# Optimization experiments

Hardware: AMD Instinct MI355X
Metric: run time of the kernel (lower is better)

Reference implementation:

```python
import jax, jax.numpy as jnp
import numpy as np

N_NODES = 100000
N_EDGES = 3200000
N_GRAPHS = 2048
DIM = 32
FEAT = 78
OUT = 128
BN_EPS = 1e-5


def setup_inputs() -> dict:
    key = jax.random.key(0)
    ks = jax.random.split(key, 16)
    x = jax.random.normal(ks[0], (N_NODES, FEAT), dtype=jnp.float32)
    edge_index = jax.random.randint(ks[1], (2, N_EDGES), 0, N_NODES, dtype=jnp.int64)
    batch = jnp.sort(jax.random.randint(ks[2], (N_NODES,), 0, N_GRAPHS, dtype=jnp.int64))
    s = 0.1
    # layer 1 MLP (78 -> 32 -> 32)
    W1a = jax.random.normal(ks[3], (FEAT, DIM), dtype=jnp.float32) * s
    b1a = jnp.zeros((DIM,), jnp.float32)
    W1b = jax.random.normal(ks[4], (DIM, DIM), dtype=jnp.float32) * s
    b1b = jnp.zeros((DIM,), jnp.float32)
    # layers 2-5 MLPs stacked (32 -> 32 -> 32)
    Wa = jax.random.normal(ks[5], (4, DIM, DIM), dtype=jnp.float32) * s
    ba = jnp.zeros((4, DIM), jnp.float32)
    Wb = jax.random.normal(ks[6], (4, DIM, DIM), dtype=jnp.float32) * s
    bb = jnp.zeros((4, DIM), jnp.float32)
    # batchnorm affine params for 5 layers
    gamma = jnp.ones((5, DIM), jnp.float32)
    beta = jnp.zeros((5, DIM), jnp.float32)
    # final graph-level linear 32 -> 128
    Wfc = jax.random.normal(ks[7], (DIM, OUT), dtype=jnp.float32) * s
    bfc = jnp.zeros((OUT,), jnp.float32)
    return {"x": x, "edge_index": edge_index, "batch": batch,
            "W1a": W1a, "b1a": b1a, "W1b": W1b, "b1b": b1b,
            "Wa": Wa, "ba": ba, "Wb": Wb, "bb": bb,
            "gamma": gamma, "beta": beta, "Wfc": Wfc, "bfc": bfc}


def _gin_layer(h, edge_index, Wa, ba, Wb, bb, g, b):
    # GIN aggregation (eps=0): h_i + sum_{j->i} h_j via scatter-add on dst
    src, dst = edge_index[0], edge_index[1]
    agg = h + jax.ops.segment_sum(h[src], dst, num_segments=h.shape[0])
    # tiny MLP: Linear -> ReLU -> Linear
    h = jax.nn.relu(agg @ Wa + ba) @ Wb + bb
    h = jax.nn.relu(h)
    # BatchNorm1d (training mode, biased variance)
    mu = h.mean(axis=0)
    var = ((h - mu) ** 2).mean(axis=0)
    return (h - mu) * jax.lax.rsqrt(var + BN_EPS) * g + b


def reference(x, edge_index, batch, W1a, b1a, W1b, b1b, Wa, ba, Wb, bb, gamma, beta, Wfc, bfc):
    h = _gin_layer(x, edge_index, W1a, b1a, W1b, b1b, gamma[0], beta[0])
    for i in range(4):
        h = _gin_layer(h, edge_index, Wa[i], ba[i], Wb[i], bb[i], gamma[i + 1], beta[i + 1])
    # global_add_pool over graphs
    pooled = jax.ops.segment_sum(h, batch, num_segments=N_GRAPHS)  # [G, 32]
    out = jax.nn.relu(pooled @ Wfc + bfc)  # dropout = identity in eval
    return out
```

## Files before the change

### kernel.cpp

```cpp
#include <hip/hip_runtime.h>
#include <hip/hip_fp16.h>

#define N_NODES 100000
#define N_GRAPHS 2048
#define N_EDGES 3200000
#define NHALF 50000
#define DIM 32
#define FEAT 78
#define OUT_DIM 128
#define BN_EPS 1e-5f

#define BSHIFT 9
#define BSIZE 512
#define NB ((N_NODES + BSIZE - 1) / BSIZE)
#define CHUNK 4096
#define NSUB 4
#define NR 4

#define NTILES (N_NODES / 16)
#define SBINS 64
#define AGG_BLOCKS 3128

typedef _Float16 f16x8 __attribute__((ext_vector_type(8)));
typedef float f32x4 __attribute__((ext_vector_type(4)));

__global__ __launch_bounds__(256) void bucket_hist_kernel(const int* __restrict__ dst,
                                                          int* __restrict__ bcnt) {
    __shared__ int lh[256];
    int tid = threadIdx.x;
    lh[tid] = 0;
    __syncthreads();
    const int4* d4 = (const int4*)dst;
    const int n4 = N_EDGES / 4;
    int i = blockIdx.x * blockDim.x + tid;
    int stride = gridDim.x * blockDim.x;
    for (; i < n4; i += stride) {
        int4 v = d4[i];
        atomicAdd(&lh[v.x >> BSHIFT], 1);
        atomicAdd(&lh[v.y >> BSHIFT], 1);
        atomicAdd(&lh[v.z >> BSHIFT], 1);
        atomicAdd(&lh[v.w >> BSHIFT], 1);
    }
    __syncthreads();
    if (tid < NB && lh[tid])
        atomicAdd(&bcnt[tid], lh[tid]);
}

__global__ __launch_bounds__(256) void bucket_scan_kernel(const int* __restrict__ bcnt,
                                                          int* __restrict__ bstart,
                                                          int* __restrict__ bcursor,
                                                          int* __restrict__ rowst) {
    __shared__ int sc[256];
    int tid = threadIdx.x;
    int v = (tid < NB) ? bcnt[tid] : 0;
    sc[tid] = v;
    __syncthreads();
    for (int off = 1; off < 256; off <<= 1) {
        int nv = (tid >= off) ? sc[tid - off] : 0;
        __syncthreads();
        sc[tid] += nv;
        __syncthreads();
    }
    if (tid < NB) {
        int ex = sc[tid] - v;
        bstart[tid] = ex;
        bcursor[tid] = ex;
    }
    if (tid == 0) {
        bstart[NB] = N_EDGES;
        rowst[N_NODES] = N_EDGES;
    }
}

__global__ __launch_bounds__(256) void bucket_scatter_kernel(const int* __restrict__ src,
                                                             const int* __restrict__ dst,
                                                             int* __restrict__ bcursor,
                                                             int* __restrict__ epk) {
    __shared__ int lpk[CHUNK];
    __shared__ unsigned char lbkt[CHUNK];
    __shared__ int lhist[4 * 256];
    __shared__ int lwcur[4 * 256];
    __shared__ int sc[256];
    __shared__ int lpre[256];
    __shared__ int gbase[256];
    int tid = threadIdx.x;
    int wave = tid >> 6;
    int base = blockIdx.x * CHUNK;
    int n = N_EDGES - base; if (n > CHUNK) n = CHUNK;

    for (int j = tid; j < 4 * 256; j += 256) lhist[j] = 0;
    __syncthreads();
    for (int i = tid; i < n; i += 256)
        atomicAdd(&lhist[wave * 256 + (dst[base + i] >> BSHIFT)], 1);
    __syncthreads();
    int c0 = lhist[0 * 256 + tid];
    int c1 = lhist[1 * 256 + tid];
    int c2 = lhist[2 * 256 + tid];
    int c3 = lhist[3 * 256 + tid];
    int v = c0 + c1 + c2 + c3;
    sc[tid] = v;
    __syncthreads();
    for (int off = 1; off < 256; off <<= 1) {
        int nv = (tid >= off) ? sc[tid - off] : 0;
        __syncthreads();
        sc[tid] += nv;
        __syncthreads();
    }
    int ex = sc[tid] - v;
    lpre[tid] = ex;
    lwcur[0 * 256 + tid] = ex;
    lwcur[1 * 256 + tid] = ex + c0;
    lwcur[2 * 256 + tid] = ex + c0 + c1;
    lwcur[3 * 256 + tid] = ex + c0 + c1 + c2;
    if (tid < NB && v)
        gbase[tid] = atomicAdd(&bcursor[tid], v);
    __syncthreads();
    for (int i = tid; i < n; i += 256) {
        int d = dst[base + i];
        int s = src[base + i];
        int b = d >> BSHIFT;
        int pos = atomicAdd(&lwcur[wave * 256 + b], 1);
        lpk[pos] = ((d & (BSIZE - 1)) << 17) | s;
        lbkt[pos] = (unsigned char)b;
    }
    __syncthreads();
    for (int i = tid; i < n; i += 256) {
        int b = lbkt[i];
        int gpos = gbase[b] + (i - lpre[b]);
        epk[gpos] = lpk[i];
    }
}

__global__ __launch_bounds__(256) void node_count_kernel(const int* __restrict__ bstart,
                                                         const int* __restrict__ epk,
                                                         int* __restrict__ qcnt) {
    __shared__ int lcnt[4 * BSIZE];
    int tid = threadIdx.x;
    int wave = tid >> 6;
    int b = blockIdx.x / NSUB;
    int qt = blockIdx.x % NSUB;
    int ss = bstart[b], se = bstart[b + 1];
    int len = se - ss;
    int qs = ss + (int)(((long long)len * qt) / NSUB);
    int qe = ss + (int)(((long long)len * (qt + 1)) / NSUB);
    for (int j = tid; j < 4 * BSIZE; j += 256) lcnt[j] = 0;
    __syncthreads();
    for (int i = qs + tid; i < qe; i += 256) {
        int pk = epk[i];
        int add = 0x10000 | (((pk & 0x1FFFF) < NHALF) ? 1 : 0);
        atomicAdd(&lcnt[wave * BSIZE + (pk >> 17)], add);
    }
    __syncthreads();
    int* qc = qcnt + (size_t)blockIdx.x * BSIZE;
    qc[tid] = lcnt[tid] + lcnt[BSIZE + tid] + lcnt[2 * BSIZE + tid] + lcnt[3 * BSIZE + tid];
    int t2 = tid + 256;
    qc[t2] = lcnt[t2] + lcnt[BSIZE + t2] + lcnt[2 * BSIZE + t2] + lcnt[3 * BSIZE + t2];
}

__global__ __launch_bounds__(256) void node_scan_kernel(const int* __restrict__ bstart,
                                                        const int* __restrict__ qcnt,
                                                        int* __restrict__ qbase0,
                                                        int* __restrict__ qbase1,
                                                        int* __restrict__ rowst,
                                                        int* __restrict__ rowmid,
                                                        float* __restrict__ degf) {
    __shared__ int sc[256];
    int tid = threadIdx.x;
    int b = blockIdx.x;
    int ss = bstart[b];
    const int* qc = qcnt + (size_t)b * NSUB * BSIZE;
    int j0 = 2 * tid, j1 = 2 * tid + 1;
    int pk0[NSUB], pk1[NSUB];
    int t0 = 0, t1 = 0, m0 = 0, m1 = 0;
    #pragma unroll
    for (int q = 0; q < NSUB; ++q) {
        pk0[q] = qc[q * BSIZE + j0];
        pk1[q] = qc[q * BSIZE + j1];
        t0 += pk0[q] >> 16; m0 += pk0[q] & 0xFFFF;
        t1 += pk1[q] >> 16; m1 += pk1[q] & 0xFFFF;
    }
    int s = t0 + t1;
    sc[tid] = s;
    __syncthreads();
    for (int off = 1; off < 256; off <<= 1) {
        int nv = (tid >= off) ? sc[tid - off] : 0;
        __syncthreads();
        sc[tid] += nv;
        __syncthreads();
    }
    int ex = sc[tid] - s;
    int B0 = ss + ex;
    int B1 = B0 + t0;
    int node_base = b << BSHIFT;
    if (node_base + j0 < N_NODES) {
        rowst[node_base + j0] = B0; rowmid[node_base + j0] = B0 + m0;
        degf[node_base + j0] = (float)(t0 + 1);
    }
    if (node_base + j1 < N_NODES) {
        rowst[node_base + j1] = B1; rowmid[node_base + j1] = B1 + m1;
        degf[node_base + j1] = (float)(t1 + 1);
    }
    int r0a = B0, r0b = B0 + m0;
    int r1a = B1, r1b = B1 + m1;
    #pragma unroll
    for (int q = 0; q < NSUB; ++q) {
        int c0 = pk0[q] & 0xFFFF, ct = pk0[q] >> 16;
        qbase0[((size_t)b * NSUB + q) * BSIZE + j0] = r0a; r0a += c0;
        qbase1[((size_t)b * NSUB + q) * BSIZE + j0] = r0b; r0b += ct - c0;
        int d0c = pk1[q] & 0xFFFF, dt = pk1[q] >> 16;
        qbase0[((size_t)b * NSUB + q) * BSIZE + j1] = r1a; r1a += d0c;
        qbase1[((size_t)b * NSUB + q) * BSIZE + j1] = r1b; r1b += dt - d0c;
    }
}

__global__ __launch_bounds__(256) void node_scatter_kernel(const int* __restrict__ bstart,
                                                           const int* __restrict__ epk,
                                                           const int* __restrict__ qbase0,
                                                           const int* __restrict__ qbase1,
                                                           int* __restrict__ csr) {
    __shared__ int lcur[2 * NSUB * 128];
    int tid = threadIdx.x;
    int b = blockIdx.x / NR;
    int r = blockIdx.x % NR;
    for (int j = tid; j < NSUB * 128; j += 256) {
        int q = j >> 7, n = j & 127;
        lcur[j] = qbase0[((size_t)b * NSUB + q) * BSIZE + r * 128 + n];
        lcur[NSUB * 128 + j] = qbase1[((size_t)b * NSUB + q) * BSIZE + r * 128 + n];
    }
    __syncthreads();
    int ss = bstart[b], se = bstart[b + 1];
    int len = se - ss;
    #pragma unroll
    for (int q = 0; q < NSUB; ++q) {
        int qs = ss + (int)(((long long)len * q) / NSUB);
        int qe = ss + (int)(((long long)len * (q + 1)) / NSUB);
        for (int i = qs + tid; i < qe; i += 256) {
            int pk = epk[i];
            int nloc = pk >> 17;
            if ((nloc >> 7) == r) {
                int s = pk & 0x1FFFF;
                int h = (s >= NHALF) ? NSUB * 128 : 0;
                int pos = atomicAdd(&lcur[h + (q << 7) + (nloc & 127)], 1);
                csr[pos] = s;
            }
        }
    }
}

__global__ __launch_bounds__(1024) void prep0_kernel(const float* __restrict__ W1a,
                                                     const float* __restrict__ W1b,
                                                     __half* __restrict__ blob1,
                                                     __half* __restrict__ blob,
                                                     float* __restrict__ cwf) {
    int tid = threadIdx.x;
    for (int idx = tid; idx < 6 * 512; idx += 1024) {
        int e = idx & 7;
        int l = (idx >> 3) & 63;
        int f = idx >> 9;
        int kc = f >> 1, ct = f & 1;
        int k = kc * 32 + (l >> 4) * 8 + e;
        int col = ct * 16 + (l & 15);
        float v = (k < FEAT) ? W1a[k * DIM + col] : 0.f;
        blob1[idx] = __float2half(v);
    }
    int d = tid >> 5, k = tid & 31;
    blob[d * 32 + k] = __float2half((d == k) ? 1.f : 0.f);
    blob[1024 + d * 32 + k] = __float2half(W1b[k * 32 + d]);
    if (tid < DIM) cwf[tid] = 0.f;
}

__global__ __launch_bounds__(256) void transform1_kernel(const float* __restrict__ x,
                                                         const __half* __restrict__ blob1,
                                                         __half* __restrict__ T) {
    __shared__ __align__(16) _Float16 X[4][512];
    int tid = threadIdx.x;
    int wave = tid >> 6;
    int l = tid & 63;
    int d0 = l & 15, kg = l >> 4;
    int tile = blockIdx.x * 4 + wave;
    if (tile >= NTILES) return;
    int tb = tile * 16;
    const float* xr = x + (size_t)(tb + d0) * FEAT;

    f16x8 af0, af1, af2;
    #pragma unroll
    for (int j = 0; j < 4; ++j) {
        int k0 = kg * 8 + 2 * j;
        float2 v0 = *(const float2*)(xr + k0);
        float2 v1 = *(const float2*)(xr + 32 + k0);
        af0[2 * j] = (_Float16)v0.x; af0[2 * j + 1] = (_Float16)v0.y;
        af1[2 * j] = (_Float16)v1.x; af1[2 * j + 1] = (_Float16)v1.y;
        int k2 = 64 + k0;
        float2 v2 = {0.f, 0.f};
        if (k2 < FEAT) v2 = *(const float2*)(xr + k2);
        af2[2 * j] = (_Float16)v2.x; af2[2 * j + 1] = (_Float16)v2.y;
    }
    f16x8 b0 = *(const f16x8*)(blob1 + (0 * 64 + l) * 8);
    f16x8 b1 = *(const f16x8*)(blob1 + (1 * 64 + l) * 8);
    f16x8 b2 = *(const f16x8*)(blob1 + (2 * 64 + l) * 8);
    f16x8 b3 = *(const f16x8*)(blob1 + (3 * 64 + l) * 8);
    f16x8 b4 = *(const f16x8*)(blob1 + (4 * 64 + l) * 8);
    f16x8 b5 = *(const f16x8*)(blob1 + (5 * 64 + l) * 8);

    f32x4 c0 = {0.f, 0.f, 0.f, 0.f};
    f32x4 c1 = {0.f, 0.f, 0.f, 0.f};
    c0 = __builtin_amdgcn_mfma_f32_16x16x32_f16(af0, b0, c0, 0, 0, 0);
    c1 = __builtin_amdgcn_mfma_f32_16x16x32_f16(af0, b1, c1, 0, 0, 0);
    c0 = __builtin_amdgcn_mfma_f32_16x16x32_f16(af1, b2, c0, 0, 0, 0);
    c1 = __builtin_amdgcn_mfma_f32_16x16x32_f16(af1, b3, c1, 0, 0, 0);
    c0 = __builtin_amdgcn_mfma_f32_16x16x32_f16(af2, b4, c0, 0, 0, 0);
    c1 = __builtin_amdgcn_mfma_f32_16x16x32_f16(af2, b5, c1, 0, 0, 0);

    #pragma unroll
    for (int rr = 0; rr < 4; ++rr) {
        int row = kg * 4 + rr;
        X[wave][row * 32 + d0] = (_Float16)c0[rr];
        X[wave][row * 32 + d0 + 16] = (_Float16)c1[rr];
    }
    __builtin_amdgcn_wave_barrier();
    int gg = l >> 2, cq = l & 3;
    uint4 vv = *(uint4*)&X[wave][gg * 32 + cq * 8];
    *(uint4*)(T + (size_t)(tb + gg) * DIM + cq * 8) = vv;
}

__global__ __launch_bounds__(1024) void prep_kernel(const float* __restrict__ sbins,
                                                    const float* __restrict__ gamma,
                                                    const float* __restrict__ beta,
                                                    const float* __restrict__ Wa,
                                                    const float* __restrict__ Wb,
                                                    __half* __restrict__ blob,
                                                    float* __restrict__ cwf) {
    __shared__ float st[64];
    __shared__ float a[DIM], c[DIM];
    int tid = threadIdx.x;
    if (tid < 64) {
        float s = 0.f;
        for (int b = 0; b < SBINS; ++b) s += sbins[b * 64 + tid];
        st[tid] = s;
    }
    __syncthreads();
    if (tid < DIM) {
        float mu = st[tid] * (1.f / N_NODES);
        float var = st[DIM + tid] * (1.f / N_NODES) - mu * mu;
        float av = gamma[tid] * rsqrtf(var + BN_EPS);
        a[tid] = av;
        c[tid] = beta[tid] - mu * av;
    }
    __syncthreads();
    int d = tid >> 5, k = tid & 31;
    blob[d * 32 + k] = __float2half(a[k] * Wa[k * 32 + d]);
    blob[1024 + d * 32 + k] = __float2half(Wb[k * 32 + d]);
    if (tid < DIM) {
        float s = 0.f;
        for (int kk = 0; kk < DIM; ++kk)
            s += c[kk] * Wa[kk * 32 + tid];
        cwf[tid] = s;
    }
}

#define ACC8(v) do { const __half2* hp_ = (const __half2*)&(v); float2 f_; \
  f_ = __half22float2(hp_[0]); a0 += f_.x; a1 += f_.y; \
  f_ = __half22float2(hp_[1]); a2 += f_.x; a3 += f_.y; \
  f_ = __half22float2(hp_[2]); a4 += f_.x; a5 += f_.y; \
  f_ = __half22float2(hp_[3]); a6 += f_.x; a7 += f_.y; } while (0)

__global__ __launch_bounds__(256) void agg_pass_kernel(const __half* __restrict__ T,
                                                       const int* __restrict__ rowst,
                                                       const int* __restrict__ rowmid,
                                                       const int* __restrict__ csr,
                                                       __half* __restrict__ P0,
                                                       __half* __restrict__ P1) {
    int b = blockIdx.x;
    int half = (b >> 2) & 1;
    int idx_in_half = (b >> 3) * 4 + (b & 3);
    int tid = threadIdx.x;
    int wave = tid >> 6;
    int l = tid & 63;
    int g = l >> 2, q = l & 3;
    int tile = idx_in_half * 4 + wave;
    if (tile >= NTILES) return;
    int node = tile * 16 + g;
    int ps, pe;
    if (half == 0) { ps = rowst[node]; pe = rowmid[node]; }
    else           { ps = rowmid[node]; pe = rowst[node + 1]; }
    float a0 = 0.f, a1 = 0.f, a2 = 0.f, a3 = 0.f,
          a4 = 0.f, a5 = 0.f, a6 = 0.f, a7 = 0.f;
    int p = ps;
    int idx[8];
    bool have = (p + 8 <= pe);
    if (have) {
        #pragma unroll
        for (int j = 0; j < 8; ++j) idx[j] = csr[p + j];
    }
    while (have) {
        uint4 v[8];
        #pragma unroll
        for (int j = 0; j < 8; ++j)
            v[j] = *(const uint4*)(T + (size_t)idx[j] * DIM + (q << 3));
        int np = p + 8;
        bool nhave = (np + 8 <= pe);
        int nidx[8];
        if (nhave) {
            #pragma unroll
            for (int j = 0; j < 8; ++j) nidx[j] = csr[np + j];
        }
        #pragma unroll
        for (int j = 0; j < 8; ++j) ACC8(v[j]);
        #pragma unroll
        for (int j = 0; j < 8; ++j) idx[j] = nidx[j];
        p = np;
        have = nhave;
    }
    if (p < pe) {
        #pragma unroll
        for (int j = 0; j < 8; ++j) {
            int ei = p + j;
            uint4 vv = {0, 0, 0, 0};
            if (ei < pe) vv = *(const uint4*)(T + (size_t)csr[ei] * DIM + (q << 3));
            ACC8(vv);
        }
    }
    int selfhalf = (node < NHALF) ? 0 : 1;
    if (selfhalf == half) {
        uint4 vs = *(const uint4*)(T + (size_t)node * DIM + (q << 3));
        ACC8(vs);
    }
    __half* P = half ? P1 : P0;
    f16x8 hv;
    hv[0] = (_Float16)a0; hv[1] = (_Float16)a1;
    hv[2] = (_Float16)a2; hv[3] = (_Float16)a3;
    hv[4] = (_Float16)a4; hv[5] = (_Float16)a5;
    hv[6] = (_Float16)a6; hv[7] = (_Float16)a7;
    *(f16x8*)(P + (size_t)node * DIM + (q << 3)) = hv;
}

__global__ __launch_bounds__(256) void mlp_kernel(const __half* __restrict__ P0,
                                                  const __half* __restrict__ P1,
                                                  const float* __restrict__ degf,
                                                  const __half* __restrict__ blob,
                                                  const float* __restrict__ cwf,
                                                  const float* __restrict__ bias_a,
                                                  const float* __restrict__ bias_b,
                                                  __half* __restrict__ outT,
                                                  float* __restrict__ sbins) {
    __shared__ __align__(16) _Float16 X[4][512];
    int tid = threadIdx.x;
    int wave = tid >> 6;
    int l = tid & 63;
    int d0 = l & 15, kg = l >> 4;
    int tile = blockIdx.x * 4 + wave;
    if (tile >= NTILES) return;
    int tb = tile * 16;

    f16x8 v0 = *(const f16x8*)(P0 + (size_t)(tb + d0) * DIM + kg * 8);
    f16x8 v1 = *(const f16x8*)(P1 + (size_t)(tb + d0) * DIM + kg * 8);
    f16x8 af = v0 + v1;
    f16x8 bA0 = *(const f16x8*)(blob + d0 * 32 + kg * 8);
    f16x8 bA1 = *(const f16x8*)(blob + (d0 + 16) * 32 + kg * 8);
    f16x8 bB0 = *(const f16x8*)(blob + 1024 + d0 * 32 + kg * 8);
    f16x8 bB1 = *(const f16x8*)(blob + 1024 + (d0 + 16) * 32 + kg * 8);
    f32x4 degv = *(const f32x4*)(degf + tb + kg * 4);
    float cw0 = cwf[d0], cw1 = cwf[d0 + 16];
    float ba0 = bias_a[d0], ba1 = bias_a[d0 + 16];
    float bb0 = bias_b[d0], bb1 = bias_b[d0 + 16];

    f32x4 c0 = {ba0, ba0, ba0, ba0};
    f32x4 c1 = {ba1, ba1, ba1, ba1};
    c0 = __builtin_amdgcn_mfma_f32_16x16x32_f16(af, bA0, c0, 0, 0, 0);
    c1 = __builtin_amdgcn_mfma_f32_16x16x32_f16(af, bA1, c1, 0, 0, 0);
    #pragma unroll
    for (int rr = 0; rr < 4; ++rr) {
        float w0 = fmaxf(c0[rr] + degv[rr] * cw0, 0.f);
        float w1 = fmaxf(c1[rr] + degv[rr] * cw1, 0.f);
        int row = kg * 4 + rr;
        X[wave][row * 32 + d0] = (_Float16)w0;
        X[wave][row * 32 + d0 + 16] = (_Float16)w1;
    }
    __builtin_amdgcn_wave_barrier();
    f16x8 af2 = *(f16x8*)&X[wave][d0 * 32 + kg * 8];
    __builtin_amdgcn_wave_barrier();

    f32x4 e0 = {bb0, bb0, bb0, bb0};
    f32x4 e1 = {bb1, bb1, bb1, bb1};
    e0 = __builtin_amdgcn_mfma_f32_16x16x32_f16(af2, bB0, e0, 0, 0, 0);
    e1 = __builtin_amdgcn_mfma_f32_16x16x32_f16(af2, bB1, e1, 0, 0, 0);
    float s0 = 0.f, ss0 = 0.f, s1 = 0.f, ss1 = 0.f;
    #pragma unroll
    for (int rr = 0; rr < 4; ++rr) {
        float y0 = fmaxf(e0[rr], 0.f);
        float y1 = fmaxf(e1[rr], 0.f);
        s0 += y0; ss0 += y0 * y0;
        s1 += y1; ss1 += y1 * y1;
        int row = kg * 4 + rr;
        X[wave][row * 32 + d0] = (_Float16)y0;
        X[wave][row * 32 + d0 + 16] = (_Float16)y1;
    }
    __builtin_amdgcn_wave_barrier();
    {
        int gg = l >> 2, c = l & 3;
        uint4 vv = *(uint4*)&X[wave][gg * 32 + c * 8];
        *(uint4*)(outT + (size_t)(tb + gg) * DIM + c * 8) = vv;
    }
    s0 += __shfl_xor(s0, 16); s0 += __shfl_xor(s0, 32);
    ss0 += __shfl_xor(ss0, 16); ss0 += __shfl_xor(ss0, 32);
    s1 += __shfl_xor(s1, 16); s1 += __shfl_xor(s1, 32);
    ss1 += __shfl_xor(ss1, 16); ss1 += __shfl_xor(ss1, 32);
    if (kg == 0) {
        float* sb = sbins + ((blockIdx.x * 4 + wave) & (SBINS - 1)) * 64;
        atomicAdd(&sb[d0], s0);
        atomicAdd(&sb[DIM + d0], ss0);
        atomicAdd(&sb[d0 + 16], s1);
        atomicAdd(&sb[DIM + d0 + 16], ss1);
    }
}

#define POOL_BLOCKS 512
__global__ __launch_bounds__(256) void bn_pool_kernel(const __half* __restrict__ h,
                                                      const float* __restrict__ sbins,
                                                      const float* __restrict__ gamma,
                                                      const float* __restrict__ beta,
                                                      const int* __restrict__ batch,
                                                      float* __restrict__ pooled) {
    __shared__ float st[64];
    int tid = threadIdx.x;
    if (tid < 64) {
        float s = 0.f;
        for (int b = 0; b < SBINS; ++b) s += sbins[b * 64 + tid];
        st[tid] = s;
    }
    __syncthreads();
    int lane = tid & 31;
    int group = tid >> 5;
    float mu = st[lane] * (1.f / N_NODES);
    float var = st[DIM + lane] * (1.f / N_NODES) - mu * mu;
    float inv = rsqrtf(var + BN_EPS);
    float a = gamma[lane] * inv;
    float c = beta[lane] - mu * a;
    const int ngroups = POOL_BLOCKS * 8;
    const int chunk = (N_NODES + ngroups - 1) / ngroups;
    int g = blockIdx.x * 8 + group;
    int start = g * chunk;
    if (start >= N_NODES) return;
    int end = start + chunk; if (end > N_NODES) end = N_NODES;
    int cur = batch[start];
    float s = 0.f;
    for (int node = start; node < end; ++node) {
        float v = __half2float(h[(size_t)node * DIM + lane]) * a + c;
        int bg = batch[node];
        if (bg != cur) {
            atomicAdd(&pooled[cur * DIM + lane], s);
            s = 0.f;
            cur = bg;
        }
        s += v;
    }
    atomicAdd(&pooled[cur * DIM + lane], s);
}

__global__ __launch_bounds__(256) void fc_kernel(const float* __restrict__ pooled,
                                                 const float* __restrict__ Wfc,
                                                 const float* __restrict__ bfc,
                                                 float* __restrict__ out) {
    __shared__ float Wl[DIM * OUT_DIM];
    for (int i = threadIdx.x; i < DIM * OUT_DIM; i += blockDim.x) Wl[i] = Wfc[i];
    __syncthreads();
    int idx = blockIdx.x * blockDim.x + threadIdx.x;
    int stride = gridDim.x * blockDim.x;
    for (; idx < N_GRAPHS * OUT_DIM; idx += stride) {
        int g = idx >> 7;
        int o = idx & 127;
        float acc = bfc[o];
        #pragma unroll
        for (int k = 0; k < DIM; ++k)
            acc += pooled[g * DIM + k] * Wl[k * OUT_DIM + o];
        out[idx] = fmaxf(acc, 0.f);
    }
}

extern "C" void kernel_launch(void* const* d_in, const int* in_sizes, int n_in,
                              void* d_out, int out_size, void* d_ws, size_t ws_size,
                              hipStream_t stream) {
    const float* x   = (const float*)d_in[0];
    const int* eidx  = (const int*)d_in[1];
    const int* src   = eidx;
    const int* dst   = eidx + N_EDGES;
    const int* batch = (const int*)d_in[2];
    const float* W1a = (const float*)d_in[3];
    const float* b1a = (const float*)d_in[4];
    const float* W1b = (const float*)d_in[5];
    const float* b1b = (const float*)d_in[6];
    const float* Wa  = (const float*)d_in[7];
    const float* ba  = (const float*)d_in[8];
    const float* Wb  = (const float*)d_in[9];
    const float* bb  = (const float*)d_in[10];
    const float* gamma = (const float*)d_in[11];
    const float* beta  = (const float*)d_in[12];
    const float* Wfc = (const float*)d_in[13];
    const float* bfc = (const float*)d_in[14];
    float* out = (float*)d_out;

    const size_t TSZ = (size_t)N_NODES * DIM;
    __half* TA = (__half*)d_ws;
    __half* TB = TA + TSZ;
    __half* P0 = TB + TSZ;
    __half* P1 = P0 + TSZ;
    float* degf   = (float*)(P1 + TSZ);
    float* sbins  = degf + N_NODES;
    float* pooled = sbins + 5 * SBINS * 64;
    float* cwf    = pooled + N_GRAPHS * DIM;
    __half* blobs = (__half*)(cwf + 5 * 32);
    __half* blob1 = blobs + 5 * 2048;
    int* csr      = (int*)(blob1 + 6 * 512);
    int* rowst    = csr + N_EDGES;
    int* rowmid   = rowst + N_NODES + 1;
    int* bcnt     = rowmid + N_NODES;
    int* bstart   = bcnt + 256;
    int* bcursor  = bstart + NB + 1;
    int* qcnt     = bcursor + 256;

    int* epk             = (int*)TA;
    int* qbase0          = (int*)P1;
    int* qbase1          = qbase0 + NB * NSUB * BSIZE;

    hipMemsetAsync(bcnt, 0, 256 * sizeof(int), stream);
    hipMemsetAsync(sbins, 0, (5 * SBINS * 64 + N_GRAPHS * DIM) * sizeof(float), stream);

    bucket_hist_kernel<<<1024, 256, 0, stream>>>(dst, bcnt);
    bucket_scan_kernel<<<1, 256, 0, stream>>>(bcnt, bstart, bcursor, rowst);
    bucket_scatter_kernel<<<(N_EDGES + CHUNK - 1) / CHUNK, 256, 0, stream>>>(src, dst, bcursor, epk);
    node_count_kernel<<<NB * NSUB, 256, 0, stream>>>(bstart, epk, qcnt);
    node_scan_kernel<<<NB, 256, 0, stream>>>(bstart, qcnt, qbase0, qbase1, rowst, rowmid, degf);
    node_scatter_kernel<<<NB * NR, 256, 0, stream>>>(bstart, epk, qbase0, qbase1, csr);

    prep0_kernel<<<1, 1024, 0, stream>>>(W1a, W1b, blob1, blobs, cwf);
    transform1_kernel<<<(NTILES + 3) / 4, 256, 0, stream>>>(x, blob1, TA);

    const __half* in = TA;
    __half* o = TB;

    agg_pass_kernel<<<AGG_BLOCKS, 256, 0, stream>>>(in, rowst, rowmid, csr, P0, P1);
    mlp_kernel<<<(NTILES + 3) / 4, 256, 0, stream>>>(P0, P1, degf, blobs, cwf, b1a, b1b, o, sbins);
    { const __half* t = in; in = o; o = (__half*)t; }

    for (int i = 0; i < 4; ++i) {
        __half* blob_i = blobs + (i + 1) * 2048;
        float* cwf_i = cwf + (i + 1) * 32;
        prep_kernel<<<1, 1024, 0, stream>>>(sbins + i * SBINS * 64, gamma + i * DIM, beta + i * DIM,
                                            Wa + i * DIM * DIM, Wb + i * DIM * DIM, blob_i, cwf_i);
        agg_pass_kernel<<<AGG_BLOCKS, 256, 0, stream>>>(in, rowst, rowmid, csr, P0, P1);
        mlp_kernel<<<(NTILES + 3) / 4, 256, 0, stream>>>(P0, P1, degf, blob_i, cwf_i,
                                                         ba + i * DIM, bb + i * DIM, o,
                                                         sbins + (i + 1) * SBINS * 64);
        { const __half* t = in; in = o; o = (__half*)t; }
    }

    bn_pool_kernel<<<POOL_BLOCKS, 256, 0, stream>>>(in, sbins + 4 * SBINS * 64,
                                                    gamma + 4 * DIM, beta + 4 * DIM, batch, pooled);
    fc_kernel<<<1024, 256, 0, stream>>>(pooled, Wfc, bfc, out);
}
```

Before: 353.9 us.

## Make edge bucketing deterministic via per-chunk histograms and batch MLP tiles per wave

Edge bucketing now writes a histogram per chunk and runs a column-wise exclusive scan per bucket. Each scatter block therefore gets precomputed global offsets instead of claiming them with global atomics on a shared cursor. This also drops the bcnt memset and the cursor array, at the cost of one extra kernel launch and a chunk-by-bucket histogram buffer. Separately, each MLP wave now handles four 16-row tiles, which amortizes weight and bias loads and cuts the BN-stat atomics, but lowers the number of waves in flight.

```diff
diff --git a/kernel.cpp b/kernel.cpp
--- a/kernel.cpp
+++ b/kernel.cpp
@@ -14,6 +14,7 @@
 #define BSIZE 512
 #define NB ((N_NODES + BSIZE - 1) / BSIZE)
 #define CHUNK 4096
+#define NCH ((N_EDGES + CHUNK - 1) / CHUNK)
 #define NSUB 4
 #define NR 4
 
@@ -25,30 +26,60 @@
 typedef float f32x4 __attribute__((ext_vector_type(4)));
 
 __global__ __launch_bounds__(256) void bucket_hist_kernel(const int* __restrict__ dst,
-                                                          int* __restrict__ bcnt) {
-    __shared__ int lh[256];
-    int tid = threadIdx.x;
-    lh[tid] = 0;
-    __syncthreads();
-    const int4* d4 = (const int4*)dst;
-    const int n4 = N_EDGES / 4;
-    int i = blockIdx.x * blockDim.x + tid;
-    int stride = gridDim.x * blockDim.x;
-    for (; i < n4; i += stride) {
+                                                          int* __restrict__ bhist) {
+    __shared__ int lh[4 * 256];
+    int tid = threadIdx.x;
+    int wave = tid >> 6;
+    for (int j = tid; j < 4 * 256; j += 256) lh[j] = 0;
+    __syncthreads();
+    int base = blockIdx.x * CHUNK;
+    int n = N_EDGES - base; if (n > CHUNK) n = CHUNK;
+    const int4* d4 = (const int4*)(dst + base);
+    for (int i = tid; i < (n >> 2); i += 256) {
         int4 v = d4[i];
-        atomicAdd(&lh[v.x >> BSHIFT], 1);
-        atomicAdd(&lh[v.y >> BSHIFT], 1);
-        atomicAdd(&lh[v.z >> BSHIFT], 1);
-        atomicAdd(&lh[v.w >> BSHIFT], 1);
-    }
-    __syncthreads();
-    if (tid < NB && lh[tid])
-        atomicAdd(&bcnt[tid], lh[tid]);
+        atomicAdd(&lh[wave * 256 + (v.x >> BSHIFT)], 1);
+        atomicAdd(&lh[wave * 256 + (v.y >> BSHIFT)], 1);
+        atomicAdd(&lh[wave * 256 + (v.z >> BSHIFT)], 1);
+        atomicAdd(&lh[wave * 256 + (v.w >> BSHIFT)], 1);
+    }
+    __syncthreads();
+    bhist[(size_t)blockIdx.x * 256 + tid] =
+        lh[tid] + lh[256 + tid] + lh[512 + tid] + lh[768 + tid];
+}
+
+__global__ __launch_bounds__(256) void col_scan_kernel(int* __restrict__ bhist,
+                                                       int* __restrict__ bcnt) {
+    __shared__ int sc[256];
+    int b = blockIdx.x;
+    int tid = threadIdx.x;
+    const int per = (NCH + 255) / 256;
+    int vals[(NCH + 255) / 256];
+    int s = 0;
+    #pragma unroll
+    for (int k = 0; k < per; ++k) {
+        int i = tid * per + k;
+        int v = (i < NCH) ? bhist[(size_t)i * 256 + b] : 0;
+        vals[k] = v; s += v;
+    }
+    sc[tid] = s;
+    __syncthreads();
+    for (int off = 1; off < 256; off <<= 1) {
+        int nv = (tid >= off) ? sc[tid - off] : 0;
+        __syncthreads();
+        sc[tid] += nv;
+        __syncthreads();
+    }
+    int run = sc[tid] - s;
+    #pragma unroll
+    for (int k = 0; k < per; ++k) {
+        int i = tid * per + k;
+        if (i < NCH) { int v = vals[k]; bhist[(size_t)i * 256 + b] = run; run += v; }
+    }
+    if (tid == 255) bcnt[b] = sc[255];
 }
 
 __global__ __launch_bounds__(256) void bucket_scan_kernel(const int* __restrict__ bcnt,
                                                           int* __restrict__ bstart,
-                                                          int* __restrict__ bcursor,
                                                           int* __restrict__ rowst) {
     __shared__ int sc[256];
     int tid = threadIdx.x;
@@ -61,11 +92,7 @@
         sc[tid] += nv;
         __syncthreads();
     }
-    if (tid < NB) {
-        int ex = sc[tid] - v;
-        bstart[tid] = ex;
-        bcursor[tid] = ex;
-    }
+    if (tid < NB) bstart[tid] = sc[tid] - v;
     if (tid == 0) {
         bstart[NB] = N_EDGES;
         rowst[N_NODES] = N_EDGES;
@@ -74,7 +101,8 @@
 
 __global__ __launch_bounds__(256) void bucket_scatter_kernel(const int* __restrict__ src,
                                                              const int* __restrict__ dst,
-                                                             int* __restrict__ bcursor,
+                                                             const int* __restrict__ bstart,
+                                                             const int* __restrict__ bhist,
                                                              int* __restrict__ epk) {
     __shared__ int lpk[CHUNK];
     __shared__ unsigned char lbkt[CHUNK];
@@ -89,6 +117,7 @@
     int n = N_EDGES - base; if (n > CHUNK) n = CHUNK;
 
     for (int j = tid; j < 4 * 256; j += 256) lhist[j] = 0;
+    gbase[tid] = ((tid < NB) ? bstart[tid] : 0) + bhist[(size_t)blockIdx.x * 256 + tid];
     __syncthreads();
     for (int i = tid; i < n; i += 256)
         atomicAdd(&lhist[wave * 256 + (dst[base + i] >> BSHIFT)], 1);
@@ -112,8 +141,6 @@
     lwcur[1 * 256 + tid] = ex + c0;
     lwcur[2 * 256 + tid] = ex + c0 + c1;
     lwcur[3 * 256 + tid] = ex + c0 + c1 + c2;
-    if (tid < NB && v)
-        gbase[tid] = atomicAdd(&bcursor[tid], v);
     __syncthreads();
     for (int i = tid; i < n; i += 256) {
         int d = dst[base + i];
@@ -434,6 +461,7 @@
     *(f16x8*)(P + (size_t)node * DIM + (q << 3)) = hv;
 }
 
+#define MLP_TPW 4
 __global__ __launch_bounds__(256) void mlp_kernel(const __half* __restrict__ P0,
                                                   const __half* __restrict__ P1,
                                                   const float* __restrict__ degf,
@@ -448,58 +476,65 @@
     int wave = tid >> 6;
     int l = tid & 63;
     int d0 = l & 15, kg = l >> 4;
-    int tile = blockIdx.x * 4 + wave;
-    if (tile >= NTILES) return;
-    int tb = tile * 16;
-
-    f16x8 v0 = *(const f16x8*)(P0 + (size_t)(tb + d0) * DIM + kg * 8);
-    f16x8 v1 = *(const f16x8*)(P1 + (size_t)(tb + d0) * DIM + kg * 8);
-    f16x8 af = v0 + v1;
+    int tbase = (blockIdx.x * 4 + wave) * MLP_TPW;
+    if (tbase >= NTILES) return;
+
     f16x8 bA0 = *(const f16x8*)(blob + d0 * 32 + kg * 8);
     f16x8 bA1 = *(const f16x8*)(blob + (d0 + 16) * 32 + kg * 8);
     f16x8 bB0 = *(const f16x8*)(blob + 1024 + d0 * 32 + kg * 8);
     f16x8 bB1 = *(const f16x8*)(blob + 1024 + (d0 + 16) * 32 + kg * 8);
-    f32x4 degv = *(const f32x4*)(degf + tb + kg * 4);
     float cw0 = cwf[d0], cw1 = cwf[d0 + 16];
     float ba0 = bias_a[d0], ba1 = bias_a[d0 + 16];
     float bb0 = bias_b[d0], bb1 = bias_b[d0 + 16];
-
-    f32x4 c0 = {ba0, ba0, ba0, ba0};
-    f32x4 c1 = {ba1, ba1, ba1, ba1};
-    c0 = __builtin_amdgcn_mfma_f32_16x16x32_f16(af, bA0, c0, 0, 0, 0);
-    c1 = __builtin_amdgcn_mfma_f32_16x16x32_f16(af, bA1, c1, 0, 0, 0);
-    #pragma unroll
-    for (int rr = 0; rr < 4; ++rr) {
-        float w0 = fmaxf(c0[rr] + degv[rr] * cw0, 0.f);
-        float w1 = fmaxf(c1[rr] + degv[rr] * cw1, 0.f);
-        int row = kg * 4 + rr;
-        X[wave][row * 32 + d0] = (_Float16)w0;
-        X[wave][row * 32 + d0 + 16] = (_Float16)w1;
-    }
-    __builtin_amdgcn_wave_barrier();
-    f16x8 af2 = *(f16x8*)&X[wave][d0 * 32 + kg * 8];
-    __builtin_amdgcn_wave_barrier();
-
-    f32x4 e0 = {bb0, bb0, bb0, bb0};
-    f32x4 e1 = {bb1, bb1, bb1, bb1};
-    e0 = __builtin_amdgcn_mfma_f32_16x16x32_f16(af2, bB0, e0, 0, 0, 0);
-    e1 = __builtin_amdgcn_mfma_f32_16x16x32_f16(af2, bB1, e1, 0, 0, 0);
     float s0 = 0.f, ss0 = 0.f, s1 = 0.f, ss1 = 0.f;
-    #pragma unroll
-    for (int rr = 0; rr < 4; ++rr) {
-        float y0 = fmaxf(e0[rr], 0.f);
-        float y1 = fmaxf(e1[rr], 0.f);
-        s0 += y0; ss0 += y0 * y0;
-        s1 += y1; ss1 += y1 * y1;
-        int row = kg * 4 + rr;
-        X[wave][row * 32 + d0] = (_Float16)y0;
-        X[wave][row * 32 + d0 + 16] = (_Float16)y1;
-    }
-    __builtin_amdgcn_wave_barrier();
-    {
-        int gg = l >> 2, c = l & 3;
-        uint4 vv = *(uint4*)&X[wave][gg * 32 + c * 8];
-        *(uint4*)(outT + (size_t)(tb + gg) * DIM + c * 8) = vv;
+
+    #pragma unroll
+    for (int it = 0; it < MLP_TPW; ++it) {
+        int tile = tbase + it;
+        if (tile >= NTILES) break;
+        int tb = tile * 16;
+        f16x8 v0 = *(const f16x8*)(P0 + (size_t)(tb + d0) * DIM + kg * 8);
+        f16x8 v1 = *(const f16x8*)(P1 + (size_t)(tb + d0) * DIM + kg * 8);
+        f16x8 af = v0 + v1;
+        f32x4 degv = *(const f32x4*)(degf + tb + kg * 4);
+
+        f32x4 c0 = {ba0, ba0, ba0, ba0};
+        f32x4 c1 = {ba1, ba1, ba1, ba1};
+        c0 = __builtin_amdgcn_mfma_f32_16x16x32_f16(af, bA0, c0, 0, 0, 0);
+        c1 = __builtin_amdgcn_mfma_f32_16x16x32_f16(af, bA1, c1, 0, 0, 0);
+        #pragma unroll
+        for (int rr = 0; rr < 4; ++rr) {
+            float w0 = fmaxf(c0[rr] + degv[rr] * cw0, 0.f);
+            float w1 = fmaxf(c1[rr] + degv[rr] * cw1, 0.f);
+            int row = kg * 4 + rr;
+            X[wave][row * 32 + d0] = (_Float16)w0;
+            X[wave][row * 32 + d0 + 16] = (_Float16)w1;
+        }
+        __builtin_amdgcn_wave_barrier();
+        f16x8 af2 = *(f16x8*)&X[wave][d0 * 32 + kg * 8];
+        __builtin_amdgcn_wave_barrier();
+
+        f32x4 e0 = {bb0, bb0, bb0, bb0};
+        f32x4 e1 = {bb1, bb1, bb1, bb1};
+        e0 = __builtin_amdgcn_mfma_f32_16x16x32_f16(af2, bB0, e0, 0, 0, 0);
+        e1 = __builtin_amdgcn_mfma_f32_16x16x32_f16(af2, bB1, e1, 0, 0, 0);
+        #pragma unroll
+        for (int rr = 0; rr < 4; ++rr) {
+            float y0 = fmaxf(e0[rr], 0.f);
+            float y1 = fmaxf(e1[rr], 0.f);
+            s0 += y0; ss0 += y0 * y0;
+            s1 += y1; ss1 += y1 * y1;
+            int row = kg * 4 + rr;
+            X[wave][row * 32 + d0] = (_Float16)y0;
+            X[wave][row * 32 + d0 + 16] = (_Float16)y1;
+        }
+        __builtin_amdgcn_wave_barrier();
+        {
+            int gg = l >> 2, c = l & 3;
+            uint4 vv = *(uint4*)&X[wave][gg * 32 + c * 8];
+            *(uint4*)(outT + (size_t)(tb + gg) * DIM + c * 8) = vv;
+        }
+        __builtin_amdgcn_wave_barrier();
     }
     s0 += __shfl_xor(s0, 16); s0 += __shfl_xor(s0, 32);
     ss0 += __shfl_xor(ss0, 16); ss0 += __shfl_xor(ss0, 32);
@@ -615,19 +650,19 @@
     int* rowmid   = rowst + N_NODES + 1;
     int* bcnt     = rowmid + N_NODES;
     int* bstart   = bcnt + 256;
-    int* bcursor  = bstart + NB + 1;
-    int* qcnt     = bcursor + 256;
+    int* qcnt     = bstart + NB + 1;
+    int* bhist    = qcnt + NB * NSUB * BSIZE;
 
     int* epk             = (int*)TA;
     int* qbase0          = (int*)P1;
     int* qbase1          = qbase0 + NB * NSUB * BSIZE;
 
-    hipMemsetAsync(bcnt, 0, 256 * sizeof(int), stream);
     hipMemsetAsync(sbins, 0, (5 * SBINS * 64 + N_GRAPHS * DIM) * sizeof(float), stream);
 
-    bucket_hist_kernel<<<1024, 256, 0, stream>>>(dst, bcnt);
-    bucket_scan_kernel<<<1, 256, 0, stream>>>(bcnt, bstart, bcursor, rowst);
-    bucket_scatter_kernel<<<(N_EDGES + CHUNK - 1) / CHUNK, 256, 0, stream>>>(src, dst, bcursor, epk);
+    bucket_hist_kernel<<<NCH, 256, 0, stream>>>(dst, bhist);
+    col_scan_kernel<<<NB, 256, 0, stream>>>(bhist, bcnt);
+    bucket_scan_kernel<<<1, 256, 0, stream>>>(bcnt, bstart, rowst);
+    bucket_scatter_kernel<<<NCH, 256, 0, stream>>>(src, dst, bstart, bhist, epk);
     node_count_kernel<<<NB * NSUB, 256, 0, stream>>>(bstart, epk, qcnt);
     node_scan_kernel<<<NB, 256, 0, stream>>>(bstart, qcnt, qbase0, qbase1, rowst, rowmid, degf);
     node_scatter_kernel<<<NB * NR, 256, 0, stream>>>(bstart, epk, qbase0, qbase1, csr);
@@ -637,9 +672,10 @@
 
     const __half* in = TA;
     __half* o = TB;
+    const int MLP_GRID = (NTILES + 4 * MLP_TPW - 1) / (4 * MLP_TPW);
 
     agg_pass_kernel<<<AGG_BLOCKS, 256, 0, stream>>>(in, rowst, rowmid, csr, P0, P1);
-    mlp_kernel<<<(NTILES + 3) / 4, 256, 0, stream>>>(P0, P1, degf, blobs, cwf, b1a, b1b, o, sbins);
+    mlp_kernel<<<MLP_GRID, 256, 0, stream>>>(P0, P1, degf, blobs, cwf, b1a, b1b, o, sbins);
     { const __half* t = in; in = o; o = (__half*)t; }
 
     for (int i = 0; i < 4; ++i) {
@@ -648,9 +684,9 @@
         prep_kernel<<<1, 1024, 0, stream>>>(sbins + i * SBINS * 64, gamma + i * DIM, beta + i * DIM,
                                             Wa + i * DIM * DIM, Wb + i * DIM * DIM, blob_i, cwf_i);
         agg_pass_kernel<<<AGG_BLOCKS, 256, 0, stream>>>(in, rowst, rowmid, csr, P0, P1);
-        mlp_kernel<<<(NTILES + 3) / 4, 256, 0, stream>>>(P0, P1, degf, blob_i, cwf_i,
-                                                         ba + i * DIM, bb + i * DIM, o,
-                                                         sbins + (i + 1) * SBINS * 64);
+        mlp_kernel<<<MLP_GRID, 256, 0, stream>>>(P0, P1, degf, blob_i, cwf_i,
+                                                 ba + i * DIM, bb + i * DIM, o,
+                                                 sbins + (i + 1) * SBINS * 64);
         { const __half* t = in; in = o; o = (__half*)t; }
     }
 
```

New measurement: 309.2 us. 12.6% less time.
